# Performance work log

Hardware: AMD Instinct MI355X
Metric: run time of the kernel (lower is better)

Reference implementation:

```python
import jax, jax.numpy as jnp
import numpy as np

N_EMBD = 1024
N_HEAD = 16
D_K = N_EMBD // N_HEAD
B, T = 2, 2048
NEG = -10000000000.0


def setup_inputs() -> dict:
    key = jax.random.key(0)
    ks = jax.random.split(key, 9)
    s = 1.0 / np.sqrt(N_EMBD)
    mk = lambda k: jax.random.uniform(k, (N_EMBD, N_EMBD), jnp.float32, -s, s)
    mb = lambda k: jax.random.uniform(k, (N_EMBD,), jnp.float32, -s, s)
    return {
        "x": jax.random.normal(ks[0], (B, T, N_EMBD), jnp.float32),
        "Wq": mk(ks[1]), "bq": mb(ks[2]),
        "Wk": mk(ks[3]), "bk": mb(ks[4]),
        "Wv": mk(ks[5]), "bv": mb(ks[6]),
        "Wo": mk(ks[7]), "bo": mb(ks[8]),
    }


def reference(x, Wq, bq, Wk, bk, Wv, bv, Wo, bo):
    Bx, Tx, _ = x.shape
    split = lambda h: h.reshape(Bx, Tx, N_HEAD, D_K).transpose(0, 2, 1, 3)  # [B,H,T,d_k]
    q = split(x @ Wq.T + bq)
    k = split(x @ Wk.T + bk)
    v = split(x @ Wv.T + bv)
    scores = jnp.einsum("bhqd,bhkd->bhqk", q, k) / np.sqrt(D_K)
    causal = jnp.tril(jnp.ones((Tx, Tx), dtype=bool))
    scores = jnp.where(causal[None, None], scores, NEG)
    prob = jax.nn.softmax(scores, axis=-1)
    y = jnp.einsum("bhqk,bhkd->bhqd", prob, v)
    y = y.transpose(0, 2, 1, 3).reshape(Bx, Tx, N_EMBD)
    return y @ Wo.T + bo
```

## Files before the change

### kernel.cpp

```cpp
#include <hip/hip_runtime.h>
#include <hip/hip_bf16.h>

#define N_EMBD 1024
#define T_SEQ  2048
#define BATCH  2
#define NHEAD  16
#define DKH    64
#define MTOK   (BATCH * T_SEQ)

typedef __attribute__((ext_vector_type(8))) short short8;
typedef __attribute__((ext_vector_type(4))) short short4v;
typedef __attribute__((ext_vector_type(4))) float floatx4;

#define QSCALE 0.18033688011112042f

static __device__ __forceinline__ short bf16_of(float f) {
    union { float f; unsigned u; } x; x.f = f;
    unsigned r = (x.u + 0x7fff + ((x.u >> 16) & 1)) >> 16;
    return (short)r;
}

static __device__ __forceinline__ void async_copy16(const void* g, void* l) {
    __builtin_amdgcn_global_load_lds(
        (const __attribute__((address_space(1))) void*)g,
        (__attribute__((address_space(3))) void*)l,
        16, 0, 0);
}

__global__ __launch_bounds__(256) void cvt_all(
    const float* __restrict__ x,  const float* __restrict__ Wq,
    const float* __restrict__ Wk, const float* __restrict__ Wv,
    const float* __restrict__ Wo,
    short* __restrict__ xb, short* __restrict__ Wqkvb, short* __restrict__ Wob) {
    int b = blockIdx.x;
    const float* src; short* dst; long base;
    if (b < 4096) { src = x; dst = xb; base = (long)b * 1024; }
    else {
        int r   = (b - 4096) >> 10;
        base    = (long)((b - 4096) & 1023) * 1024;
        if (r == 0)      { src = Wq; dst = Wqkvb;           }
        else if (r == 1) { src = Wk; dst = Wqkvb + 1048576; }
        else if (r == 2) { src = Wv; dst = Wqkvb + 2097152; }
        else             { src = Wo; dst = Wob;             }
    }
    long i = base + threadIdx.x * 4;
    float4 v = *(const float4*)(src + i);
    short4 o;
    o.x = bf16_of(v.x); o.y = bf16_of(v.y); o.z = bf16_of(v.z); o.w = bf16_of(v.w);
    *(short4*)(dst + i) = o;
}

template<int MODE>
__global__ __launch_bounds__(256) void gemm_bt(
    const short* __restrict__ A, const short* __restrict__ Bw,
    const float* __restrict__ b0, const float* __restrict__ b1, const float* __restrict__ b2,
    short* __restrict__ outQ, short* __restrict__ outK, short* __restrict__ outV,
    float* __restrict__ outP, int K)
{
    constexpr int TM = (MODE == 0) ? 128 : 64;
    constexpr int NI = TM / 32;
    __shared__ short As[TM * 32];
    __shared__ short Bs[128 * 32];
    const int tid  = threadIdx.x;
    const int w    = tid >> 6, lane = tid & 63;
    const int quad = lane >> 4, lr = lane & 15;
    const int wm   = (w & 1) * (TM / 2), wn = (w >> 1) * 64;
    const long m0  = (long)blockIdx.y * TM, n0 = (long)blockIdx.x * 128;

    floatx4 acc[NI][4] = {};

    const int srow = lane >> 2;
    const int scol = (lane & 3) * 8;
    const short* gA = A  + (m0 + w * 16 + srow) * (long)K + scol;
    const short* gB = Bw + (n0 + w * 16 + srow) * (long)K + scol;

    for (int kt = 0; kt < K; kt += 32) {
        async_copy16(gA + kt,            As + w * 512);
        if (TM == 128) async_copy16(gA + kt + 64L * K,  As + (w + 4) * 512);
        async_copy16(gB + kt,            Bs + w * 512);
        async_copy16(gB + kt + 64L * K,  Bs + (w + 4) * 512);
        __syncthreads();

        const short8* As8 = (const short8*)As;
        const short8* Bs8 = (const short8*)Bs;
        short8 af[NI], bf[4];
#pragma unroll
        for (int i = 0; i < NI; ++i) af[i] = As8[(wm + i * 16 + lr) * 4 + quad];
#pragma unroll
        for (int j = 0; j < 4; ++j) bf[j] = Bs8[(wn + j * 16 + lr) * 4 + quad];
#pragma unroll
        for (int i = 0; i < NI; ++i)
#pragma unroll
            for (int j = 0; j < 4; ++j)
                acc[i][j] = __builtin_amdgcn_mfma_f32_16x16x32_bf16(af[i], bf[j], acc[i][j], 0, 0, 0);
        __syncthreads();
    }

#pragma unroll
    for (int i = 0; i < NI; ++i) {
#pragma unroll
        for (int j = 0; j < 4; ++j) {
#pragma unroll
            for (int r = 0; r < 4; ++r) {
                long m = m0 + wm + i * 16 + quad * 4 + r;
                long n = n0 + wn + j * 16 + lr;
                float v = acc[i][j][r];
                if (MODE == 0) {
                    int sel = (int)(n >> 10);
                    int nn  = (int)(n & 1023);
                    v += (sel == 0 ? b0[nn] : (sel == 1 ? b1[nn] : b2[nn]));
                    int  h  = nn >> 6, d = nn & 63;
                    int  t  = (int)(m & 2047);
                    long bh = (m >> 11) * NHEAD + h;
                    if (sel == 2) {
                        long idx = (((long)bh * 64 + (t >> 5)) * 4 + (d >> 4)) * 512
                                 + (((t >> 2) & 3) * 16 + (d & 15)) * 8
                                 + ((t >> 4) & 1) * 4 + (t & 3);
                        outV[idx] = bf16_of(v);
                    } else {
                        long idx = (((long)bh * 128 + (t >> 4)) * 2 + (d >> 5)) * 512
                                 + (((d >> 3) & 3) * 16 + (t & 15)) * 8 + (d & 7);
                        if (sel == 0) outQ[idx] = bf16_of(v * QSCALE);
                        else          outK[idx] = bf16_of(v);
                    }
                } else {
                    v += b0[(int)n];
                    outP[m * N_EMBD + n] = v;
                }
            }
        }
    }
}

__global__ __launch_bounds__(256) void attn_kernel(
    const short* __restrict__ Qf, const short* __restrict__ Kf,
    const short* __restrict__ Vf, short* __restrict__ Y)
{
    __shared__ float Ob[2][32][68];
    __shared__ float Lb[2][32];

    const int tid  = threadIdx.x;
    const int w    = tid >> 6, lane = tid & 63;
    const int quad = lane >> 4, lr = lane & 15;
    const int qs   = w & 1, half = w >> 1;

    const int id = blockIdx.x;
    const int bh = id & 31;
    const int pr = id >> 5;

    const short* Qp = Qf + (long)bh * 131072;
    const short* Kp = Kf + (long)bh * 131072;
    const short* Vp = Vf + (long)bh * 131072;

    const long trow_base = (long)(bh >> 4) * T_SEQ;
    const int  hcol      = (bh & 15) * DKH;

    for (int ph = 0; ph < 2; ++ph) {
        const int qt  = ph ? (31 - pr) : pr;
        const int qrb = qt * 64 + qs * 32;
        const int qb  = qrb >> 4;

        short8 qfv[2][2];
#pragma unroll
        for (int m = 0; m < 2; ++m)
#pragma unroll
            for (int c = 0; c < 2; ++c)
                qfv[m][c] = *(const short8*)(Qp + (long)(((qb + m) * 2 + c) * 512) + lane * 8);

        floatx4 o[2][4] = {};
        float rs[2] = {0.f, 0.f};

        const int S_tot = 2 * qt + qs + 1;
        const int h0 = (S_tot + 1) >> 1;
        const int sb = half ? h0 : 0;
        const int se = half ? S_tot : h0;

        short8 kbn[2][2];
        if (sb < se) {
#pragma unroll
            for (int blk = 0; blk < 2; ++blk)
#pragma unroll
                for (int c = 0; c < 2; ++c)
                    kbn[blk][c] = *(const short8*)(Kp + (long)(((sb * 2 + blk) * 2 + c) * 512) + lane * 8);
        }

        for (int s = sb; s < se; ++s) {
            short8 ka[2][2];
#pragma unroll
            for (int blk = 0; blk < 2; ++blk)
#pragma unroll
                for (int c = 0; c < 2; ++c) ka[blk][c] = kbn[blk][c];
            if (s + 1 < se) {
#pragma unroll
                for (int blk = 0; blk < 2; ++blk)
#pragma unroll
                    for (int c = 0; c < 2; ++c)
                        kbn[blk][c] = *(const short8*)(Kp + (long)((((s + 1) * 2 + blk) * 2 + c) * 512) + lane * 8);
            }
            short8 va[4];
#pragma unroll
            for (int d = 0; d < 4; ++d)
                va[d] = *(const short8*)(Vp + (long)((s * 4 + d) * 512) + lane * 8);

            floatx4 sc[2][2];
#pragma unroll
            for (int m = 0; m < 2; ++m)
#pragma unroll
                for (int blk = 0; blk < 2; ++blk) {
                    floatx4 z = {};
                    z = __builtin_amdgcn_mfma_f32_16x16x32_bf16(ka[blk][0], qfv[m][0], z, 0, 0, 0);
                    z = __builtin_amdgcn_mfma_f32_16x16x32_bf16(ka[blk][1], qfv[m][1], z, 0, 0, 0);
                    sc[m][blk] = z;
                }

            if (s == S_tot - 1) {
                const int k0 = s * 32;
#pragma unroll
                for (int m = 0; m < 2; ++m)
#pragma unroll
                    for (int blk = 0; blk < 2; ++blk)
#pragma unroll
                        for (int r = 0; r < 4; ++r) {
                            int key = k0 + blk * 16 + quad * 4 + r;
                            if (key > qrb + m * 16 + lr) sc[m][blk][r] = -INFINITY;
                        }
            }

            short8 pa[2];
#pragma unroll
            for (int m = 0; m < 2; ++m) {
                union { short8 v; short e[8]; } pu;
#pragma unroll
                for (int blk = 0; blk < 2; ++blk)
#pragma unroll
                    for (int r = 0; r < 4; ++r) {
                        float p = __builtin_amdgcn_exp2f(sc[m][blk][r]);
                        rs[m] += p;
                        union { float f; unsigned u; } cc; cc.f = p;
                        pu.e[blk * 4 + r] = (short)((cc.u + 0x8000u) >> 16);
                    }
                pa[m] = pu.v;
            }

#pragma unroll
            for (int m = 0; m < 2; ++m)
#pragma unroll
                for (int d = 0; d < 4; ++d)
                    o[m][d] = __builtin_amdgcn_mfma_f32_16x16x32_bf16(va[d], pa[m], o[m][d], 0, 0, 0);
        }

#pragma unroll
        for (int m = 0; m < 2; ++m) {
            rs[m] += __shfl_xor(rs[m], 16, 64);
            rs[m] += __shfl_xor(rs[m], 32, 64);
        }

        if (half == 1) {
#pragma unroll
            for (int m = 0; m < 2; ++m) {
#pragma unroll
                for (int d = 0; d < 4; ++d)
                    *(floatx4*)&Ob[qs][m * 16 + lr][d * 16 + quad * 4] = o[m][d];
                Lb[qs][m * 16 + lr] = rs[m];
            }
        }
        __syncthreads();
        if (half == 0) {
#pragma unroll
            for (int m = 0; m < 2; ++m) {
                float l   = rs[m] + Lb[qs][m * 16 + lr];
                float inv = 1.f / l;
                long  yb  = (trow_base + qrb + m * 16 + lr) * N_EMBD + hcol;
#pragma unroll
                for (int d = 0; d < 4; ++d) {
                    floatx4 ob = *(const floatx4*)&Ob[qs][m * 16 + lr][d * 16 + quad * 4];
                    short4v y4;
#pragma unroll
                    for (int r = 0; r < 4; ++r) y4[r] = bf16_of((o[m][d][r] + ob[r]) * inv);
                    *(short4v*)(Y + yb + d * 16 + quad * 4) = y4;
                }
            }
        }
        __syncthreads();
    }
}

extern "C" void kernel_launch(void* const* d_in, const int* in_sizes, int n_in,
                              void* d_out, int out_size, void* d_ws, size_t ws_size,
                              hipStream_t stream) {
    const float* x  = (const float*)d_in[0];
    const float* Wq = (const float*)d_in[1];
    const float* bq = (const float*)d_in[2];
    const float* Wk = (const float*)d_in[3];
    const float* bk = (const float*)d_in[4];
    const float* Wv = (const float*)d_in[5];
    const float* bv = (const float*)d_in[6];
    const float* Wo = (const float*)d_in[7];
    const float* bo = (const float*)d_in[8];
    float* out = (float*)d_out;

    char* ws = (char*)d_ws;
    short* xb    = (short*)(ws);
    short* Wqkvb = (short*)(ws + (8L  << 20));
    short* Wob   = (short*)(ws + (14L << 20));
    short* Qb    = (short*)(ws + (16L << 20));
    short* Kbuf  = (short*)(ws + (24L << 20));
    short* Vtb   = (short*)(ws + (32L << 20));
    short* Yb    = xb;

    cvt_all<<<8192, 256, 0, stream>>>(x, Wq, Wk, Wv, Wo, xb, Wqkvb, Wob);

    gemm_bt<0><<<dim3(24, 32), 256, 0, stream>>>(xb, Wqkvb, bq, bk, bv,
                                                 Qb, Kbuf, Vtb, nullptr, N_EMBD);
    attn_kernel<<<512, 256, 0, stream>>>(Qb, Kbuf, Vtb, Yb);
    gemm_bt<1><<<dim3(8, 64), 256, 0, stream>>>(Yb, Wob, bo, nullptr, nullptr,
                                                nullptr, nullptr, nullptr, out, N_EMBD);
}
```

Baseline: 189.2 us.

## Swap GEMM operand roles for vectorized epilogue stores and split attention blocks

The QKV GEMM now computes the Q/K part transposed (weights as the A operand, tokens as B) and the V part untransposed. Each lane's four accumulator rows then fall on contiguous positions of the packed Q/K/V layouts, so scattered scalar bf16 stores become 8-byte vector stores. The output projection is transposed the same way so it writes float4 rows. The attention kernel drops its two-phase paired-tile loop and launches one block per query tile (1024 blocks), heaviest tiles first. This gives finer scheduling granularity, at the cost of losing the explicit balancing from pairing short and long tiles.

After: 184.1 us. -2.7%, faster.

```diff
diff --git a/kernel.cpp b/kernel.cpp
--- a/kernel.cpp
+++ b/kernel.cpp
@@ -50,84 +50,162 @@
     *(short4*)(dst + i) = o;
 }
 
-template<int MODE>
-__global__ __launch_bounds__(256) void gemm_bt(
-    const short* __restrict__ A, const short* __restrict__ Bw,
-    const float* __restrict__ b0, const float* __restrict__ b1, const float* __restrict__ b2,
-    short* __restrict__ outQ, short* __restrict__ outK, short* __restrict__ outV,
-    float* __restrict__ outP, int K)
+__global__ __launch_bounds__(256) void gemm_qkv(
+    const short* __restrict__ xb, const short* __restrict__ Wqkv,
+    const float* __restrict__ bq, const float* __restrict__ bk, const float* __restrict__ bv,
+    short* __restrict__ outQ, short* __restrict__ outK, short* __restrict__ outV)
 {
-    constexpr int TM = (MODE == 0) ? 128 : 64;
-    constexpr int NI = TM / 32;
-    __shared__ short As[TM * 32];
+    __shared__ short As[128 * 32];
     __shared__ short Bs[128 * 32];
     const int tid  = threadIdx.x;
     const int w    = tid >> 6, lane = tid & 63;
     const int quad = lane >> 4, lr = lane & 15;
-    const int wm   = (w & 1) * (TM / 2), wn = (w >> 1) * 64;
-    const long m0  = (long)blockIdx.y * TM, n0 = (long)blockIdx.x * 128;
-
-    floatx4 acc[NI][4] = {};
+    const int wm   = (w & 1) * 64, wn = (w >> 1) * 64;
+
+    const int  id   = blockIdx.x;
+    const bool isQK = id < 512;
+    long m0, n0;
+    const short *Aptr, *Bptr;
+    if (isQK) {
+        m0 = (long)(id >> 5) * 128;
+        n0 = (long)(id & 31) * 128;
+        Aptr = Wqkv;       Bptr = xb;
+    } else {
+        int v = id - 512;
+        m0 = (long)(v >> 3) * 128;
+        n0 = (long)(v & 7) * 128;
+        Aptr = xb;         Bptr = Wqkv + 2097152;
+    }
+
+    floatx4 acc[4][4] = {};
 
     const int srow = lane >> 2;
     const int scol = (lane & 3) * 8;
-    const short* gA = A  + (m0 + w * 16 + srow) * (long)K + scol;
-    const short* gB = Bw + (n0 + w * 16 + srow) * (long)K + scol;
-
-    for (int kt = 0; kt < K; kt += 32) {
-        async_copy16(gA + kt,            As + w * 512);
-        if (TM == 128) async_copy16(gA + kt + 64L * K,  As + (w + 4) * 512);
-        async_copy16(gB + kt,            Bs + w * 512);
-        async_copy16(gB + kt + 64L * K,  Bs + (w + 4) * 512);
+    const short* gA = Aptr + (m0 + w * 16 + srow) * 1024L + scol;
+    const short* gB = Bptr + (n0 + w * 16 + srow) * 1024L + scol;
+
+    for (int kt = 0; kt < 1024; kt += 32) {
+        async_copy16(gA + kt,              As + w * 512);
+        async_copy16(gA + kt + 64L * 1024, As + (w + 4) * 512);
+        async_copy16(gB + kt,              Bs + w * 512);
+        async_copy16(gB + kt + 64L * 1024, Bs + (w + 4) * 512);
         __syncthreads();
 
         const short8* As8 = (const short8*)As;
         const short8* Bs8 = (const short8*)Bs;
-        short8 af[NI], bf[4];
-#pragma unroll
-        for (int i = 0; i < NI; ++i) af[i] = As8[(wm + i * 16 + lr) * 4 + quad];
+        short8 af[4], bf[4];
+#pragma unroll
+        for (int i = 0; i < 4; ++i) af[i] = As8[(wm + i * 16 + lr) * 4 + quad];
 #pragma unroll
         for (int j = 0; j < 4; ++j) bf[j] = Bs8[(wn + j * 16 + lr) * 4 + quad];
 #pragma unroll
-        for (int i = 0; i < NI; ++i)
+        for (int i = 0; i < 4; ++i)
 #pragma unroll
             for (int j = 0; j < 4; ++j)
                 acc[i][j] = __builtin_amdgcn_mfma_f32_16x16x32_bf16(af[i], bf[j], acc[i][j], 0, 0, 0);
         __syncthreads();
     }
 
-#pragma unroll
-    for (int i = 0; i < NI; ++i) {
+    if (isQK) {
+#pragma unroll
+        for (int i = 0; i < 4; ++i) {
+#pragma unroll
+            for (int j = 0; j < 4; ++j) {
+                int f0  = (int)m0 + wm + i * 16 + quad * 4;
+                int t   = (int)n0 + wn + j * 16 + lr;
+                int tb  = t & 2047;
+                int sel = f0 >> 10;
+                int fb  = f0 & 1023;
+                int h   = fb >> 6, d0 = fb & 63;
+                long bh = (long)(t >> 11) * NHEAD + h;
+                const float* bias = sel ? bk : bq;
+                short4v y;
+#pragma unroll
+                for (int r = 0; r < 4; ++r) {
+                    float v = acc[i][j][r] + bias[fb + r];
+                    if (sel == 0) v *= QSCALE;
+                    y[r] = bf16_of(v);
+                }
+                long idx = ((bh * 128 + (tb >> 4)) * 2 + (d0 >> 5)) * 512
+                         + (((d0 >> 3) & 3) * 16 + (tb & 15)) * 8 + (d0 & 7);
+                *(short4v*)((sel ? outK : outQ) + idx) = y;
+            }
+        }
+    } else {
+#pragma unroll
+        for (int i = 0; i < 4; ++i) {
+#pragma unroll
+            for (int j = 0; j < 4; ++j) {
+                int t0 = (int)m0 + wm + i * 16 + quad * 4;
+                int tb = t0 & 2047;
+                int n  = (int)n0 + wn + j * 16 + lr;
+                int h  = n >> 6, d = n & 63;
+                long bh = (long)(t0 >> 11) * NHEAD + h;
+                float bias = bv[n];
+                short4v y;
+#pragma unroll
+                for (int r = 0; r < 4; ++r) y[r] = bf16_of(acc[i][j][r] + bias);
+                long idx = ((bh * 64 + (tb >> 5)) * 4 + (d >> 4)) * 512
+                         + (((tb >> 2) & 3) * 16 + (d & 15)) * 8 + ((tb >> 4) & 1) * 4;
+                *(short4v*)(outV + idx) = y;
+            }
+        }
+    }
+}
+
+__global__ __launch_bounds__(256) void gemm_proj(
+    const short* __restrict__ Yb, const short* __restrict__ Wo,
+    const float* __restrict__ bo, float* __restrict__ out)
+{
+    __shared__ short As[64 * 32];
+    __shared__ short Bs[128 * 32];
+    const int tid  = threadIdx.x;
+    const int w    = tid >> 6, lane = tid & 63;
+    const int quad = lane >> 4, lr = lane & 15;
+    const int wm   = (w & 1) * 32, wn = (w >> 1) * 64;
+    const long m0  = (long)blockIdx.y * 64;
+    const long n0  = (long)blockIdx.x * 128;
+
+    floatx4 acc[2][4] = {};
+
+    const int srow = lane >> 2;
+    const int scol = (lane & 3) * 8;
+    const short* gA = Wo + (m0 + w * 16 + srow) * 1024L + scol;
+    const short* gB = Yb + (n0 + w * 16 + srow) * 1024L + scol;
+
+    for (int kt = 0; kt < 1024; kt += 32) {
+        async_copy16(gA + kt,              As + w * 512);
+        async_copy16(gB + kt,              Bs + w * 512);
+        async_copy16(gB + kt + 64L * 1024, Bs + (w + 4) * 512);
+        __syncthreads();
+
+        const short8* As8 = (const short8*)As;
+        const short8* Bs8 = (const short8*)Bs;
+        short8 af[2], bf[4];
+#pragma unroll
+        for (int i = 0; i < 2; ++i) af[i] = As8[(wm + i * 16 + lr) * 4 + quad];
+#pragma unroll
+        for (int j = 0; j < 4; ++j) bf[j] = Bs8[(wn + j * 16 + lr) * 4 + quad];
+#pragma unroll
+        for (int i = 0; i < 2; ++i)
+#pragma unroll
+            for (int j = 0; j < 4; ++j)
+                acc[i][j] = __builtin_amdgcn_mfma_f32_16x16x32_bf16(af[i], bf[j], acc[i][j], 0, 0, 0);
+        __syncthreads();
+    }
+
+#pragma unroll
+    for (int i = 0; i < 2; ++i) {
 #pragma unroll
         for (int j = 0; j < 4; ++j) {
-#pragma unroll
-            for (int r = 0; r < 4; ++r) {
-                long m = m0 + wm + i * 16 + quad * 4 + r;
-                long n = n0 + wn + j * 16 + lr;
-                float v = acc[i][j][r];
-                if (MODE == 0) {
-                    int sel = (int)(n >> 10);
-                    int nn  = (int)(n & 1023);
-                    v += (sel == 0 ? b0[nn] : (sel == 1 ? b1[nn] : b2[nn]));
-                    int  h  = nn >> 6, d = nn & 63;
-                    int  t  = (int)(m & 2047);
-                    long bh = (m >> 11) * NHEAD + h;
-                    if (sel == 2) {
-                        long idx = (((long)bh * 64 + (t >> 5)) * 4 + (d >> 4)) * 512
-                                 + (((t >> 2) & 3) * 16 + (d & 15)) * 8
-                                 + ((t >> 4) & 1) * 4 + (t & 3);
-                        outV[idx] = bf16_of(v);
-                    } else {
-                        long idx = (((long)bh * 128 + (t >> 4)) * 2 + (d >> 5)) * 512
-                                 + (((d >> 3) & 3) * 16 + (t & 15)) * 8 + (d & 7);
-                        if (sel == 0) outQ[idx] = bf16_of(v * QSCALE);
-                        else          outK[idx] = bf16_of(v);
-                    }
-                } else {
-                    v += b0[(int)n];
-                    outP[m * N_EMBD + n] = v;
-                }
-            }
+            int  f0 = (int)m0 + wm + i * 16 + quad * 4;
+            long t  = n0 + wn + j * 16 + lr;
+            float4 o4;
+            o4.x = acc[i][j][0] + bo[f0 + 0];
+            o4.y = acc[i][j][1] + bo[f0 + 1];
+            o4.z = acc[i][j][2] + bo[f0 + 2];
+            o4.w = acc[i][j][3] + bo[f0 + 3];
+            *(float4*)(out + t * N_EMBD + f0) = o4;
         }
     }
 }
@@ -145,143 +223,138 @@
     const int qs   = w & 1, half = w >> 1;
 
     const int id = blockIdx.x;
+    const int qt = 31 - (id >> 5);
     const int bh = id & 31;
-    const int pr = id >> 5;
 
     const short* Qp = Qf + (long)bh * 131072;
     const short* Kp = Kf + (long)bh * 131072;
     const short* Vp = Vf + (long)bh * 131072;
 
-    const long trow_base = (long)(bh >> 4) * T_SEQ;
-    const int  hcol      = (bh & 15) * DKH;
-
-    for (int ph = 0; ph < 2; ++ph) {
-        const int qt  = ph ? (31 - pr) : pr;
-        const int qrb = qt * 64 + qs * 32;
-        const int qb  = qrb >> 4;
-
-        short8 qfv[2][2];
+    const int qrb = qt * 64 + qs * 32;
+    const int qb  = qrb >> 4;
+
+    short8 qfv[2][2];
+#pragma unroll
+    for (int m = 0; m < 2; ++m)
+#pragma unroll
+        for (int c = 0; c < 2; ++c)
+            qfv[m][c] = *(const short8*)(Qp + (long)(((qb + m) * 2 + c) * 512) + lane * 8);
+
+    floatx4 o[2][4] = {};
+    float rs[2] = {0.f, 0.f};
+
+    const int S_tot = 2 * qt + qs + 1;
+    const int h0 = (S_tot + 1) >> 1;
+    const int sb = half ? h0 : 0;
+    const int se = half ? S_tot : h0;
+
+    short8 kbn[2][2];
+    if (sb < se) {
+#pragma unroll
+        for (int blk = 0; blk < 2; ++blk)
+#pragma unroll
+            for (int c = 0; c < 2; ++c)
+                kbn[blk][c] = *(const short8*)(Kp + (long)(((sb * 2 + blk) * 2 + c) * 512) + lane * 8);
+    }
+
+    for (int s = sb; s < se; ++s) {
+        short8 ka[2][2];
+#pragma unroll
+        for (int blk = 0; blk < 2; ++blk)
+#pragma unroll
+            for (int c = 0; c < 2; ++c) ka[blk][c] = kbn[blk][c];
+        if (s + 1 < se) {
+#pragma unroll
+            for (int blk = 0; blk < 2; ++blk)
+#pragma unroll
+                for (int c = 0; c < 2; ++c)
+                    kbn[blk][c] = *(const short8*)(Kp + (long)((((s + 1) * 2 + blk) * 2 + c) * 512) + lane * 8);
+        }
+        short8 va[4];
+#pragma unroll
+        for (int d = 0; d < 4; ++d)
+            va[d] = *(const short8*)(Vp + (long)((s * 4 + d) * 512) + lane * 8);
+
+        floatx4 sc[2][2];
 #pragma unroll
         for (int m = 0; m < 2; ++m)
 #pragma unroll
-            for (int c = 0; c < 2; ++c)
-                qfv[m][c] = *(const short8*)(Qp + (long)(((qb + m) * 2 + c) * 512) + lane * 8);
-
-        floatx4 o[2][4] = {};
-        float rs[2] = {0.f, 0.f};
-
-        const int S_tot = 2 * qt + qs + 1;
-        const int h0 = (S_tot + 1) >> 1;
-        const int sb = half ? h0 : 0;
-        const int se = half ? S_tot : h0;
-
-        short8 kbn[2][2];
-        if (sb < se) {
+            for (int blk = 0; blk < 2; ++blk) {
+                floatx4 z = {};
+                z = __builtin_amdgcn_mfma_f32_16x16x32_bf16(ka[blk][0], qfv[m][0], z, 0, 0, 0);
+                z = __builtin_amdgcn_mfma_f32_16x16x32_bf16(ka[blk][1], qfv[m][1], z, 0, 0, 0);
+                sc[m][blk] = z;
+            }
+
+        if (s == S_tot - 1) {
+            const int k0 = s * 32;
+#pragma unroll
+            for (int m = 0; m < 2; ++m)
+#pragma unroll
+                for (int blk = 0; blk < 2; ++blk)
+#pragma unroll
+                    for (int r = 0; r < 4; ++r) {
+                        int key = k0 + blk * 16 + quad * 4 + r;
+                        if (key > qrb + m * 16 + lr) sc[m][blk][r] = -INFINITY;
+                    }
+        }
+
+        short8 pa[2];
+#pragma unroll
+        for (int m = 0; m < 2; ++m) {
+            union { short8 v; short e[8]; } pu;
 #pragma unroll
             for (int blk = 0; blk < 2; ++blk)
 #pragma unroll
-                for (int c = 0; c < 2; ++c)
-                    kbn[blk][c] = *(const short8*)(Kp + (long)(((sb * 2 + blk) * 2 + c) * 512) + lane * 8);
-        }
-
-        for (int s = sb; s < se; ++s) {
-            short8 ka[2][2];
-#pragma unroll
-            for (int blk = 0; blk < 2; ++blk)
-#pragma unroll
-                for (int c = 0; c < 2; ++c) ka[blk][c] = kbn[blk][c];
-            if (s + 1 < se) {
-#pragma unroll
-                for (int blk = 0; blk < 2; ++blk)
-#pragma unroll
-                    for (int c = 0; c < 2; ++c)
-                        kbn[blk][c] = *(const short8*)(Kp + (long)((((s + 1) * 2 + blk) * 2 + c) * 512) + lane * 8);
+                for (int r = 0; r < 4; ++r) {
+                    float p = __builtin_amdgcn_exp2f(sc[m][blk][r]);
+                    rs[m] += p;
+                    union { float f; unsigned u; } cc; cc.f = p;
+                    pu.e[blk * 4 + r] = (short)((cc.u + 0x8000u) >> 16);
+                }
+            pa[m] = pu.v;
+        }
+
+#pragma unroll
+        for (int m = 0; m < 2; ++m)
+#pragma unroll
+            for (int d = 0; d < 4; ++d)
+                o[m][d] = __builtin_amdgcn_mfma_f32_16x16x32_bf16(va[d], pa[m], o[m][d], 0, 0, 0);
+    }
+
+#pragma unroll
+    for (int m = 0; m < 2; ++m) {
+        rs[m] += __shfl_xor(rs[m], 16, 64);
+        rs[m] += __shfl_xor(rs[m], 32, 64);
+    }
+
+    if (half == 1) {
+#pragma unroll
+        for (int m = 0; m < 2; ++m) {
+#pragma unroll
+            for (int d = 0; d < 4; ++d)
+                *(floatx4*)&Ob[qs][m * 16 + lr][d * 16 + quad * 4] = o[m][d];
+            Lb[qs][m * 16 + lr] = rs[m];
+        }
+    }
+    __syncthreads();
+    if (half == 0) {
+        const long trow0 = (long)(bh >> 4) * T_SEQ + qrb;
+        const int  hcol  = (bh & 15) * DKH;
+#pragma unroll
+        for (int m = 0; m < 2; ++m) {
+            float l   = rs[m] + Lb[qs][m * 16 + lr];
+            float inv = 1.f / l;
+            long  yb  = (trow0 + m * 16 + lr) * N_EMBD + hcol;
+#pragma unroll
+            for (int d = 0; d < 4; ++d) {
+                floatx4 ob = *(const floatx4*)&Ob[qs][m * 16 + lr][d * 16 + quad * 4];
+                short4v y4;
+#pragma unroll
+                for (int r = 0; r < 4; ++r) y4[r] = bf16_of((o[m][d][r] + ob[r]) * inv);
+                *(short4v*)(Y + yb + d * 16 + quad * 4) = y4;
             }
-            short8 va[4];
-#pragma unroll
-            for (int d = 0; d < 4; ++d)
-                va[d] = *(const short8*)(Vp + (long)((s * 4 + d) * 512) + lane * 8);
-
-            floatx4 sc[2][2];
-#pragma unroll
-            for (int m = 0; m < 2; ++m)
-#pragma unroll
-                for (int blk = 0; blk < 2; ++blk) {
-                    floatx4 z = {};
-                    z = __builtin_amdgcn_mfma_f32_16x16x32_bf16(ka[blk][0], qfv[m][0], z, 0, 0, 0);
-                    z = __builtin_amdgcn_mfma_f32_16x16x32_bf16(ka[blk][1], qfv[m][1], z, 0, 0, 0);
-                    sc[m][blk] = z;
-                }
-
-            if (s == S_tot - 1) {
-                const int k0 = s * 32;
-#pragma unroll
-                for (int m = 0; m < 2; ++m)
-#pragma unroll
-                    for (int blk = 0; blk < 2; ++blk)
-#pragma unroll
-                        for (int r = 0; r < 4; ++r) {
-                            int key = k0 + blk * 16 + quad * 4 + r;
-                            if (key > qrb + m * 16 + lr) sc[m][blk][r] = -INFINITY;
-                        }
-            }
-
-            short8 pa[2];
-#pragma unroll
-            for (int m = 0; m < 2; ++m) {
-                union { short8 v; short e[8]; } pu;
-#pragma unroll
-                for (int blk = 0; blk < 2; ++blk)
-#pragma unroll
-                    for (int r = 0; r < 4; ++r) {
-                        float p = __builtin_amdgcn_exp2f(sc[m][blk][r]);
-                        rs[m] += p;
-                        union { float f; unsigned u; } cc; cc.f = p;
-                        pu.e[blk * 4 + r] = (short)((cc.u + 0x8000u) >> 16);
-                    }
-                pa[m] = pu.v;
-            }
-
-#pragma unroll
-            for (int m = 0; m < 2; ++m)
-#pragma unroll
-                for (int d = 0; d < 4; ++d)
-                    o[m][d] = __builtin_amdgcn_mfma_f32_16x16x32_bf16(va[d], pa[m], o[m][d], 0, 0, 0);
-        }
-
-#pragma unroll
-        for (int m = 0; m < 2; ++m) {
-            rs[m] += __shfl_xor(rs[m], 16, 64);
-            rs[m] += __shfl_xor(rs[m], 32, 64);
-        }
-
-        if (half == 1) {
-#pragma unroll
-            for (int m = 0; m < 2; ++m) {
-#pragma unroll
-                for (int d = 0; d < 4; ++d)
-                    *(floatx4*)&Ob[qs][m * 16 + lr][d * 16 + quad * 4] = o[m][d];
-                Lb[qs][m * 16 + lr] = rs[m];
-            }
-        }
-        __syncthreads();
-        if (half == 0) {
-#pragma unroll
-            for (int m = 0; m < 2; ++m) {
-                float l   = rs[m] + Lb[qs][m * 16 + lr];
-                float inv = 1.f / l;
-                long  yb  = (trow_base + qrb + m * 16 + lr) * N_EMBD + hcol;
-#pragma unroll
-                for (int d = 0; d < 4; ++d) {
-                    floatx4 ob = *(const floatx4*)&Ob[qs][m * 16 + lr][d * 16 + quad * 4];
-                    short4v y4;
-#pragma unroll
-                    for (int r = 0; r < 4; ++r) y4[r] = bf16_of((o[m][d][r] + ob[r]) * inv);
-                    *(short4v*)(Y + yb + d * 16 + quad * 4) = y4;
-                }
-            }
-        }
-        __syncthreads();
+        }
     }
 }
 
@@ -310,9 +383,7 @@
 
     cvt_all<<<8192, 256, 0, stream>>>(x, Wq, Wk, Wv, Wo, xb, Wqkvb, Wob);
 
-    gemm_bt<0><<<dim3(24, 32), 256, 0, stream>>>(xb, Wqkvb, bq, bk, bv,
-                                                 Qb, Kbuf, Vtb, nullptr, N_EMBD);
-    attn_kernel<<<512, 256, 0, stream>>>(Qb, Kbuf, Vtb, Yb);
-    gemm_bt<1><<<dim3(8, 64), 256, 0, stream>>>(Yb, Wob, bo, nullptr, nullptr,
-                                                nullptr, nullptr, nullptr, out, N_EMBD);
-}
+    gemm_qkv<<<768, 256, 0, stream>>>(xb, Wqkvb, bq, bk, bv, Qb, Kbuf, Vtb);
+    attn_kernel<<<1024, 256, 0, stream>>>(Qb, Kbuf, Vtb, Yb);
+    gemm_proj<<<dim3(32, 16), 256, 0, stream>>>(Yb, Wob, bo, out);
+}
```

## Pre-swizzle operands into MFMA fragment layout and use LDS-free single-wave GEMMs

Applied to the files above, without the earlier changes.

The conversion kernel now writes x and all weights directly in MFMA fragment order, so the GEMMs load fragments straight from global memory into registers with software double-buffering and no LDS staging or barriers. Each GEMM runs as one 64-thread wave per 64x128 tile, and Q/K are computed transposed so that bias and output stores vectorize. The attention kernel now launches one block per query tile instead of pairing two tiles per block, and it writes Y in fragment layout for the projection GEMM. The trade-off is heavy register pressure from the 4x8 accumulators, no cross-wave operand reuse in LDS, and a less balanced attention workload.

Measured after the change: 173.6 us. -8.3%, faster.

```diff
diff --git a/kernel.cpp b/kernel.cpp
--- a/kernel.cpp
+++ b/kernel.cpp
@@ -20,114 +20,162 @@
     return (short)r;
 }
 
-static __device__ __forceinline__ void async_copy16(const void* g, void* l) {
-    __builtin_amdgcn_global_load_lds(
-        (const __attribute__((address_space(1))) void*)g,
-        (__attribute__((address_space(3))) void*)l,
-        16, 0, 0);
-}
-
-__global__ __launch_bounds__(256) void cvt_all(
+
+__global__ __launch_bounds__(256) void cvt_frag(
     const float* __restrict__ x,  const float* __restrict__ Wq,
     const float* __restrict__ Wk, const float* __restrict__ Wv,
     const float* __restrict__ Wo,
-    short* __restrict__ xb, short* __restrict__ Wqkvb, short* __restrict__ Wob) {
+    short* __restrict__ xf, short* __restrict__ wqkf,
+    short* __restrict__ wvf, short* __restrict__ wof)
+{
     int b = blockIdx.x;
-    const float* src; short* dst; long base;
-    if (b < 4096) { src = x; dst = xb; base = (long)b * 1024; }
-    else {
-        int r   = (b - 4096) >> 10;
-        base    = (long)((b - 4096) & 1023) * 1024;
-        if (r == 0)      { src = Wq; dst = Wqkvb;           }
-        else if (r == 1) { src = Wk; dst = Wqkvb + 1048576; }
-        else if (r == 2) { src = Wv; dst = Wqkvb + 2097152; }
-        else             { src = Wo; dst = Wob;             }
-    }
-    long i = base + threadIdx.x * 4;
-    float4 v = *(const float4*)(src + i);
-    short4 o;
-    o.x = bf16_of(v.x); o.y = bf16_of(v.y); o.z = bf16_of(v.z); o.w = bf16_of(v.w);
-    *(short4*)(dst + i) = o;
-}
-
-template<int MODE>
-__global__ __launch_bounds__(256) void gemm_bt(
-    const short* __restrict__ A, const short* __restrict__ Bw,
-    const float* __restrict__ b0, const float* __restrict__ b1, const float* __restrict__ b2,
-    short* __restrict__ outQ, short* __restrict__ outK, short* __restrict__ outV,
-    float* __restrict__ outP, int K)
+    const float* src; short* dst; int srb, drb;
+    if (b < 256)      { src = x;  dst = xf;   srb = b;       drb = srb; }
+    else if (b < 320) { src = Wq; dst = wqkf; srb = b - 256; drb = srb; }
+    else if (b < 384) { src = Wk; dst = wqkf; srb = b - 320; drb = srb + 64; }
+    else if (b < 448) { src = Wv; dst = wvf;  srb = b - 384; drb = srb; }
+    else              { src = Wo; dst = wof;  srb = b - 448; drb = srb; }
+
+    const int row16 = threadIdx.x >> 4;
+    const int kseg  = (threadIdx.x & 15) * 64;
+    const float* sp = src + ((long)srb * 16 + row16) * 1024 + kseg;
+    short* dp       = dst + ((long)drb * 32 + (kseg >> 5)) * 512 + row16 * 8;
+
+#pragma unroll
+    for (int c = 0; c < 8; ++c) {
+        float4 v0 = *(const float4*)(sp + c * 8);
+        float4 v1 = *(const float4*)(sp + c * 8 + 4);
+        short8 o;
+        o[0] = bf16_of(v0.x); o[1] = bf16_of(v0.y); o[2] = bf16_of(v0.z); o[3] = bf16_of(v0.w);
+        o[4] = bf16_of(v1.x); o[5] = bf16_of(v1.y); o[6] = bf16_of(v1.z); o[7] = bf16_of(v1.w);
+        *(short8*)(dp + (c >> 2) * 512 + (c & 3) * 128) = o;
+    }
+}
+
+#define GEMM_KLOOP(Ab, Bb)                                                     \
+    floatx4 acc[4][8] = {};                                                    \
+    short8 a0[4], a1[4], b0[8], b1[8];                                         \
+    _Pragma("unroll") for (int i = 0; i < 4; ++i)                              \
+        a0[i] = *(const short8*)(Ab + (long)i * 32 * 512);                     \
+    _Pragma("unroll") for (int j = 0; j < 8; ++j)                              \
+        b0[j] = *(const short8*)(Bb + (long)j * 32 * 512);                     \
+    for (int kc = 0; kc < 32; kc += 2) {                                       \
+        _Pragma("unroll") for (int i = 0; i < 4; ++i)                          \
+            a1[i] = *(const short8*)(Ab + ((long)i * 32 + kc + 1) * 512);      \
+        _Pragma("unroll") for (int j = 0; j < 8; ++j)                          \
+            b1[j] = *(const short8*)(Bb + ((long)j * 32 + kc + 1) * 512);      \
+        _Pragma("unroll") for (int i = 0; i < 4; ++i)                          \
+            _Pragma("unroll") for (int j = 0; j < 8; ++j)                      \
+                acc[i][j] = __builtin_amdgcn_mfma_f32_16x16x32_bf16(           \
+                    a0[i], b0[j], acc[i][j], 0, 0, 0);                         \
+        if (kc + 2 < 32) {                                                     \
+            _Pragma("unroll") for (int i = 0; i < 4; ++i)                      \
+                a0[i] = *(const short8*)(Ab + ((long)i * 32 + kc + 2) * 512);  \
+            _Pragma("unroll") for (int j = 0; j < 8; ++j)                      \
+                b0[j] = *(const short8*)(Bb + ((long)j * 32 + kc + 2) * 512);  \
+        }                                                                      \
+        _Pragma("unroll") for (int i = 0; i < 4; ++i)                          \
+            _Pragma("unroll") for (int j = 0; j < 8; ++j)                      \
+                acc[i][j] = __builtin_amdgcn_mfma_f32_16x16x32_bf16(           \
+                    a1[i], b1[j], acc[i][j], 0, 0, 0);                         \
+    }
+
+__global__ __launch_bounds__(64, 2) void gemm_qkv(
+    const short* __restrict__ xf, const short* __restrict__ wqkf,
+    const short* __restrict__ wvf,
+    const float* __restrict__ bq, const float* __restrict__ bk, const float* __restrict__ bv,
+    short* __restrict__ outQ, short* __restrict__ outK, short* __restrict__ outV)
 {
-    constexpr int TM = (MODE == 0) ? 128 : 64;
-    constexpr int NI = TM / 32;
-    __shared__ short As[TM * 32];
-    __shared__ short Bs[128 * 32];
-    const int tid  = threadIdx.x;
-    const int w    = tid >> 6, lane = tid & 63;
+    const int lane = threadIdx.x & 63;
     const int quad = lane >> 4, lr = lane & 15;
-    const int wm   = (w & 1) * (TM / 2), wn = (w >> 1) * 64;
-    const long m0  = (long)blockIdx.y * TM, n0 = (long)blockIdx.x * 128;
-
-    floatx4 acc[NI][4] = {};
-
-    const int srow = lane >> 2;
-    const int scol = (lane & 3) * 8;
-    const short* gA = A  + (m0 + w * 16 + srow) * (long)K + scol;
-    const short* gB = Bw + (n0 + w * 16 + srow) * (long)K + scol;
-
-    for (int kt = 0; kt < K; kt += 32) {
-        async_copy16(gA + kt,            As + w * 512);
-        if (TM == 128) async_copy16(gA + kt + 64L * K,  As + (w + 4) * 512);
-        async_copy16(gB + kt,            Bs + w * 512);
-        async_copy16(gB + kt + 64L * K,  Bs + (w + 4) * 512);
-        __syncthreads();
-
-        const short8* As8 = (const short8*)As;
-        const short8* Bs8 = (const short8*)Bs;
-        short8 af[NI], bf[4];
-#pragma unroll
-        for (int i = 0; i < NI; ++i) af[i] = As8[(wm + i * 16 + lr) * 4 + quad];
-#pragma unroll
-        for (int j = 0; j < 4; ++j) bf[j] = Bs8[(wn + j * 16 + lr) * 4 + quad];
-#pragma unroll
-        for (int i = 0; i < NI; ++i)
-#pragma unroll
-            for (int j = 0; j < 4; ++j)
-                acc[i][j] = __builtin_amdgcn_mfma_f32_16x16x32_bf16(af[i], bf[j], acc[i][j], 0, 0, 0);
-        __syncthreads();
-    }
-
-#pragma unroll
-    for (int i = 0; i < NI; ++i) {
-#pragma unroll
-        for (int j = 0; j < 4; ++j) {
-#pragma unroll
-            for (int r = 0; r < 4; ++r) {
-                long m = m0 + wm + i * 16 + quad * 4 + r;
-                long n = n0 + wn + j * 16 + lr;
-                float v = acc[i][j][r];
-                if (MODE == 0) {
-                    int sel = (int)(n >> 10);
-                    int nn  = (int)(n & 1023);
-                    v += (sel == 0 ? b0[nn] : (sel == 1 ? b1[nn] : b2[nn]));
-                    int  h  = nn >> 6, d = nn & 63;
-                    int  t  = (int)(m & 2047);
-                    long bh = (m >> 11) * NHEAD + h;
-                    if (sel == 2) {
-                        long idx = (((long)bh * 64 + (t >> 5)) * 4 + (d >> 4)) * 512
-                                 + (((t >> 2) & 3) * 16 + (d & 15)) * 8
-                                 + ((t >> 4) & 1) * 4 + (t & 3);
-                        outV[idx] = bf16_of(v);
-                    } else {
-                        long idx = (((long)bh * 128 + (t >> 4)) * 2 + (d >> 5)) * 512
-                                 + (((d >> 3) & 3) * 16 + (t & 15)) * 8 + (d & 7);
-                        if (sel == 0) outQ[idx] = bf16_of(v * QSCALE);
-                        else          outK[idx] = bf16_of(v);
-                    }
-                } else {
-                    v += b0[(int)n];
-                    outP[m * N_EMBD + n] = v;
+    const int wid  = blockIdx.x;
+    const bool isQK = wid < 1024;
+    int mw, nw;
+    const short *Af, *Bf;
+    if (isQK) { mw = (wid >> 5) * 64;          nw = (wid & 31) * 128; Af = wqkf; Bf = xf; }
+    else      { int v = wid - 1024;
+                mw = (v >> 3) * 64;            nw = (v & 7) * 128;    Af = xf;   Bf = wvf; }
+
+    const short* Ab = Af + (long)(mw >> 4) * 32 * 512 + lane * 8;
+    const short* Bb = Bf + (long)(nw >> 4) * 32 * 512 + lane * 8;
+
+    GEMM_KLOOP(Ab, Bb)
+
+    if (isQK) {
+#pragma unroll
+        for (int i = 0; i < 4; ++i) {
+#pragma unroll
+            for (int j = 0; j < 8; ++j) {
+                int f0  = mw + i * 16 + quad * 4;
+                int t   = nw + j * 16 + lr;
+                int tb  = t & 2047;
+                int sel = f0 >> 10;
+                int fb  = f0 & 1023;
+                int h   = fb >> 6, d0 = fb & 63;
+                long bh = (long)(t >> 11) * NHEAD + h;
+                float4 bias = *(const float4*)((sel ? bk : bq) + fb);
+                short4v y;
+#pragma unroll
+                for (int r = 0; r < 4; ++r) {
+                    float v = acc[i][j][r] + (&bias.x)[r];
+                    if (sel == 0) v *= QSCALE;
+                    y[r] = bf16_of(v);
                 }
+                long idx = ((bh * 128 + (tb >> 4)) * 2 + (d0 >> 5)) * 512
+                         + (((d0 >> 3) & 3) * 16 + (tb & 15)) * 8 + (d0 & 7);
+                *(short4v*)((sel ? outK : outQ) + idx) = y;
             }
+        }
+    } else {
+#pragma unroll
+        for (int i = 0; i < 4; ++i) {
+#pragma unroll
+            for (int j = 0; j < 8; ++j) {
+                int t0 = mw + i * 16 + quad * 4;
+                int tb = t0 & 2047;
+                int d  = nw + j * 16 + lr;
+                int h  = d >> 6, dblk = (d >> 4) & 3;
+                long bh = (long)(t0 >> 11) * NHEAD + h;
+                float bias = bv[d];
+                short4v y;
+#pragma unroll
+                for (int r = 0; r < 4; ++r) y[r] = bf16_of(acc[i][j][r] + bias);
+                long idx = ((bh * 64 + (tb >> 5)) * 4 + dblk) * 512
+                         + lane * 8 + (i & 1) * 4;
+                *(short4v*)(outV + idx) = y;
+            }
+        }
+    }
+}
+
+__global__ __launch_bounds__(64, 2) void gemm_proj(
+    const short* __restrict__ Yf, const short* __restrict__ wof,
+    const float* __restrict__ bo, float* __restrict__ out)
+{
+    const int lane = threadIdx.x & 63;
+    const int quad = lane >> 4, lr = lane & 15;
+    const int wid  = blockIdx.x;
+    const int mw   = (wid >> 5) * 64;
+    const int nw   = (wid & 31) * 128;
+
+    const short* Ab = wof + (long)(mw >> 4) * 32 * 512 + lane * 8;
+    const short* Bb = Yf  + (long)(nw >> 4) * 32 * 512 + lane * 8;
+
+    GEMM_KLOOP(Ab, Bb)
+
+#pragma unroll
+    for (int i = 0; i < 4; ++i) {
+#pragma unroll
+        for (int j = 0; j < 8; ++j) {
+            int  f0 = mw + i * 16 + quad * 4;
+            long t  = nw + j * 16 + lr;
+            float4 b4 = *(const float4*)(bo + f0);
+            float4 o4;
+            o4.x = acc[i][j][0] + b4.x;
+            o4.y = acc[i][j][1] + b4.y;
+            o4.z = acc[i][j][2] + b4.z;
+            o4.w = acc[i][j][3] + b4.w;
+            *(float4*)(out + t * N_EMBD + f0) = o4;
         }
     }
 }
@@ -145,143 +193,141 @@
     const int qs   = w & 1, half = w >> 1;
 
     const int id = blockIdx.x;
+    const int qt = 31 - (id >> 5);
     const int bh = id & 31;
-    const int pr = id >> 5;
 
     const short* Qp = Qf + (long)bh * 131072;
     const short* Kp = Kf + (long)bh * 131072;
     const short* Vp = Vf + (long)bh * 131072;
 
-    const long trow_base = (long)(bh >> 4) * T_SEQ;
-    const int  hcol      = (bh & 15) * DKH;
-
-    for (int ph = 0; ph < 2; ++ph) {
-        const int qt  = ph ? (31 - pr) : pr;
-        const int qrb = qt * 64 + qs * 32;
-        const int qb  = qrb >> 4;
-
-        short8 qfv[2][2];
+    const int qrb = qt * 64 + qs * 32;
+    const int qb  = qrb >> 4;
+
+    short8 qfv[2][2];
+#pragma unroll
+    for (int m = 0; m < 2; ++m)
+#pragma unroll
+        for (int c = 0; c < 2; ++c)
+            qfv[m][c] = *(const short8*)(Qp + (long)(((qb + m) * 2 + c) * 512) + lane * 8);
+
+    floatx4 o[2][4] = {};
+    float rs[2] = {0.f, 0.f};
+
+    const int S_tot = 2 * qt + qs + 1;
+    const int h0 = (S_tot + 1) >> 1;
+    const int sb = half ? h0 : 0;
+    const int se = half ? S_tot : h0;
+
+    short8 kbn[2][2];
+    if (sb < se) {
+#pragma unroll
+        for (int blk = 0; blk < 2; ++blk)
+#pragma unroll
+            for (int c = 0; c < 2; ++c)
+                kbn[blk][c] = *(const short8*)(Kp + (long)(((sb * 2 + blk) * 2 + c) * 512) + lane * 8);
+    }
+
+    for (int s = sb; s < se; ++s) {
+        short8 ka[2][2];
+#pragma unroll
+        for (int blk = 0; blk < 2; ++blk)
+#pragma unroll
+            for (int c = 0; c < 2; ++c) ka[blk][c] = kbn[blk][c];
+        if (s + 1 < se) {
+#pragma unroll
+            for (int blk = 0; blk < 2; ++blk)
+#pragma unroll
+                for (int c = 0; c < 2; ++c)
+                    kbn[blk][c] = *(const short8*)(Kp + (long)((((s + 1) * 2 + blk) * 2 + c) * 512) + lane * 8);
+        }
+        short8 va[4];
+#pragma unroll
+        for (int d = 0; d < 4; ++d)
+            va[d] = *(const short8*)(Vp + (long)((s * 4 + d) * 512) + lane * 8);
+
+        floatx4 sc[2][2];
 #pragma unroll
         for (int m = 0; m < 2; ++m)
 #pragma unroll
-            for (int c = 0; c < 2; ++c)
-                qfv[m][c] = *(const short8*)(Qp + (long)(((qb + m) * 2 + c) * 512) + lane * 8);
-
-        floatx4 o[2][4] = {};
-        float rs[2] = {0.f, 0.f};
-
-        const int S_tot = 2 * qt + qs + 1;
-        const int h0 = (S_tot + 1) >> 1;
-        const int sb = half ? h0 : 0;
-        const int se = half ? S_tot : h0;
-
-        short8 kbn[2][2];
-        if (sb < se) {
+            for (int blk = 0; blk < 2; ++blk) {
+                floatx4 z = {};
+                z = __builtin_amdgcn_mfma_f32_16x16x32_bf16(ka[blk][0], qfv[m][0], z, 0, 0, 0);
+                z = __builtin_amdgcn_mfma_f32_16x16x32_bf16(ka[blk][1], qfv[m][1], z, 0, 0, 0);
+                sc[m][blk] = z;
+            }
+
+        if (s == S_tot - 1) {
+            const int k0 = s * 32;
+#pragma unroll
+            for (int m = 0; m < 2; ++m)
+#pragma unroll
+                for (int blk = 0; blk < 2; ++blk)
+#pragma unroll
+                    for (int r = 0; r < 4; ++r) {
+                        int key = k0 + blk * 16 + quad * 4 + r;
+                        if (key > qrb + m * 16 + lr) sc[m][blk][r] = -INFINITY;
+                    }
+        }
+
+        short8 pa[2];
+#pragma unroll
+        for (int m = 0; m < 2; ++m) {
+            union { short8 v; short e[8]; } pu;
 #pragma unroll
             for (int blk = 0; blk < 2; ++blk)
 #pragma unroll
-                for (int c = 0; c < 2; ++c)
-                    kbn[blk][c] = *(const short8*)(Kp + (long)(((sb * 2 + blk) * 2 + c) * 512) + lane * 8);
-        }
-
-        for (int s = sb; s < se; ++s) {
-            short8 ka[2][2];
-#pragma unroll
-            for (int blk = 0; blk < 2; ++blk)
-#pragma unroll
-                for (int c = 0; c < 2; ++c) ka[blk][c] = kbn[blk][c];
-            if (s + 1 < se) {
-#pragma unroll
-                for (int blk = 0; blk < 2; ++blk)
-#pragma unroll
-                    for (int c = 0; c < 2; ++c)
-                        kbn[blk][c] = *(const short8*)(Kp + (long)((((s + 1) * 2 + blk) * 2 + c) * 512) + lane * 8);
+                for (int r = 0; r < 4; ++r) {
+                    float p = __builtin_amdgcn_exp2f(sc[m][blk][r]);
+                    rs[m] += p;
+                    union { float f; unsigned u; } cc; cc.f = p;
+                    pu.e[blk * 4 + r] = (short)((cc.u + 0x8000u) >> 16);
+                }
+            pa[m] = pu.v;
+        }
+
+#pragma unroll
+        for (int m = 0; m < 2; ++m)
+#pragma unroll
+            for (int d = 0; d < 4; ++d)
+                o[m][d] = __builtin_amdgcn_mfma_f32_16x16x32_bf16(va[d], pa[m], o[m][d], 0, 0, 0);
+    }
+
+#pragma unroll
+    for (int m = 0; m < 2; ++m) {
+        rs[m] += __shfl_xor(rs[m], 16, 64);
+        rs[m] += __shfl_xor(rs[m], 32, 64);
+    }
+
+    if (half == 1) {
+#pragma unroll
+        for (int m = 0; m < 2; ++m) {
+#pragma unroll
+            for (int d = 0; d < 4; ++d)
+                *(floatx4*)&Ob[qs][m * 16 + lr][d * 16 + quad * 4] = o[m][d];
+            Lb[qs][m * 16 + lr] = rs[m];
+        }
+    }
+    __syncthreads();
+    if (half == 0) {
+        const long rb0 = (long)(bh >> 4) * 128 + qb;
+        const int  hk  = (bh & 15) * DKH;
+#pragma unroll
+        for (int m = 0; m < 2; ++m) {
+            float l   = rs[m] + Lb[qs][m * 16 + lr];
+            float inv = 1.f / l;
+            long  rb  = rb0 + m;
+#pragma unroll
+            for (int d = 0; d < 4; ++d) {
+                floatx4 ob = *(const floatx4*)&Ob[qs][m * 16 + lr][d * 16 + quad * 4];
+                short4v y4;
+#pragma unroll
+                for (int r = 0; r < 4; ++r) y4[r] = bf16_of((o[m][d][r] + ob[r]) * inv);
+                int kb = hk + d * 16 + quad * 4;
+                long idx = (rb * 32 + (kb >> 5)) * 512
+                         + (((kb >> 3) & 3) * 16 + lr) * 8 + (quad & 1) * 4;
+                *(short4v*)(Y + idx) = y4;
             }
-            short8 va[4];
-#pragma unroll
-            for (int d = 0; d < 4; ++d)
-                va[d] = *(const short8*)(Vp + (long)((s * 4 + d) * 512) + lane * 8);
-
-            floatx4 sc[2][2];
-#pragma unroll
-            for (int m = 0; m < 2; ++m)
-#pragma unroll
-                for (int blk = 0; blk < 2; ++blk) {
-                    floatx4 z = {};
-                    z = __builtin_amdgcn_mfma_f32_16x16x32_bf16(ka[blk][0], qfv[m][0], z, 0, 0, 0);
-                    z = __builtin_amdgcn_mfma_f32_16x16x32_bf16(ka[blk][1], qfv[m][1], z, 0, 0, 0);
-                    sc[m][blk] = z;
-                }
-
-            if (s == S_tot - 1) {
-                const int k0 = s * 32;
-#pragma unroll
-                for (int m = 0; m < 2; ++m)
-#pragma unroll
-                    for (int blk = 0; blk < 2; ++blk)
-#pragma unroll
-                        for (int r = 0; r < 4; ++r) {
-                            int key = k0 + blk * 16 + quad * 4 + r;
-                            if (key > qrb + m * 16 + lr) sc[m][blk][r] = -INFINITY;
-                        }
-            }
-
-            short8 pa[2];
-#pragma unroll
-            for (int m = 0; m < 2; ++m) {
-                union { short8 v; short e[8]; } pu;
-#pragma unroll
-                for (int blk = 0; blk < 2; ++blk)
-#pragma unroll
-                    for (int r = 0; r < 4; ++r) {
-                        float p = __builtin_amdgcn_exp2f(sc[m][blk][r]);
-                        rs[m] += p;
-                        union { float f; unsigned u; } cc; cc.f = p;
-                        pu.e[blk * 4 + r] = (short)((cc.u + 0x8000u) >> 16);
-                    }
-                pa[m] = pu.v;
-            }
-
-#pragma unroll
-            for (int m = 0; m < 2; ++m)
-#pragma unroll
-                for (int d = 0; d < 4; ++d)
-                    o[m][d] = __builtin_amdgcn_mfma_f32_16x16x32_bf16(va[d], pa[m], o[m][d], 0, 0, 0);
-        }
-
-#pragma unroll
-        for (int m = 0; m < 2; ++m) {
-            rs[m] += __shfl_xor(rs[m], 16, 64);
-            rs[m] += __shfl_xor(rs[m], 32, 64);
-        }
-
-        if (half == 1) {
-#pragma unroll
-            for (int m = 0; m < 2; ++m) {
-#pragma unroll
-                for (int d = 0; d < 4; ++d)
-                    *(floatx4*)&Ob[qs][m * 16 + lr][d * 16 + quad * 4] = o[m][d];
-                Lb[qs][m * 16 + lr] = rs[m];
-            }
-        }
-        __syncthreads();
-        if (half == 0) {
-#pragma unroll
-            for (int m = 0; m < 2; ++m) {
-                float l   = rs[m] + Lb[qs][m * 16 + lr];
-                float inv = 1.f / l;
-                long  yb  = (trow_base + qrb + m * 16 + lr) * N_EMBD + hcol;
-#pragma unroll
-                for (int d = 0; d < 4; ++d) {
-                    floatx4 ob = *(const floatx4*)&Ob[qs][m * 16 + lr][d * 16 + quad * 4];
-                    short4v y4;
-#pragma unroll
-                    for (int r = 0; r < 4; ++r) y4[r] = bf16_of((o[m][d][r] + ob[r]) * inv);
-                    *(short4v*)(Y + yb + d * 16 + quad * 4) = y4;
-                }
-            }
-        }
-        __syncthreads();
+        }
     }
 }
 
@@ -300,19 +346,18 @@
     float* out = (float*)d_out;
 
     char* ws = (char*)d_ws;
-    short* xb    = (short*)(ws);
-    short* Wqkvb = (short*)(ws + (8L  << 20));
-    short* Wob   = (short*)(ws + (14L << 20));
-    short* Qb    = (short*)(ws + (16L << 20));
-    short* Kbuf  = (short*)(ws + (24L << 20));
-    short* Vtb   = (short*)(ws + (32L << 20));
-    short* Yb    = xb;
-
-    cvt_all<<<8192, 256, 0, stream>>>(x, Wq, Wk, Wv, Wo, xb, Wqkvb, Wob);
-
-    gemm_bt<0><<<dim3(24, 32), 256, 0, stream>>>(xb, Wqkvb, bq, bk, bv,
-                                                 Qb, Kbuf, Vtb, nullptr, N_EMBD);
-    attn_kernel<<<512, 256, 0, stream>>>(Qb, Kbuf, Vtb, Yb);
-    gemm_bt<1><<<dim3(8, 64), 256, 0, stream>>>(Yb, Wob, bo, nullptr, nullptr,
-                                                nullptr, nullptr, nullptr, out, N_EMBD);
-}
+    short* xf   = (short*)(ws);
+    short* wqkf = (short*)(ws + (8L  << 20));
+    short* wvf  = (short*)(ws + (12L << 20));
+    short* wof  = (short*)(ws + (14L << 20));
+    short* Qb   = (short*)(ws + (16L << 20));
+    short* Kbuf = (short*)(ws + (24L << 20));
+    short* Vtb  = (short*)(ws + (32L << 20));
+    short* Yf   = xf;
+
+    cvt_frag<<<512, 256, 0, stream>>>(x, Wq, Wk, Wv, Wo, xf, wqkf, wvf, wof);
+
+    gemm_qkv<<<1536, 64, 0, stream>>>(xf, wqkf, wvf, bq, bk, bv, Qb, Kbuf, Vtb);
+    attn_kernel<<<1024, 256, 0, stream>>>(Qb, Kbuf, Vtb, Yf);
+    gemm_proj<<<512, 64, 0, stream>>>(Yf, wof, bo, out);
+}
```
